# Kernel optimization log

Measured on AMD Instinct MI355X. Metric: run time of the kernel, lower is better.

Reference implementation:

```python
import jax, jax.numpy as jnp
import numpy as np

# Mamba-1.4B-like dims
BATCH, SEQ, HID = 1, 2048, 2048
INTER, STATE, DT_RANK, KCONV = 4096, 16, 128, 4


def setup_inputs() -> dict:
    key = jax.random.key(0)
    ks = jax.random.split(key, 8)
    f = jnp.float32
    return {
        "input_states": jax.random.normal(ks[0], (BATCH, SEQ, HID), f),
        "in_proj_w": jax.random.normal(ks[1], (HID, 2 * INTER), f) * (HID ** -0.5),
        "conv_w": jax.random.normal(ks[2], (INTER, 1, KCONV), f) * (KCONV ** -0.5),  # (O, I/groups=1, K) depthwise
        "conv_b": jnp.zeros((INTER,), f),
        "x_proj_w": jax.random.normal(ks[3], (INTER, DT_RANK + 2 * STATE), f) * (INTER ** -0.5),
        "dt_proj_w": jax.random.normal(ks[4], (DT_RANK, INTER), f) * (DT_RANK ** -0.5),
        "dt_proj_b": jax.random.normal(ks[5], (INTER,), f) * 0.1,
        "A_log": jnp.log(jnp.broadcast_to(jnp.arange(1, STATE + 1, dtype=f), (INTER, STATE))),
        "D": jnp.ones((INTER,), f),
        "out_proj_w": jax.random.normal(ks[6], (INTER, HID), f) * (INTER ** -0.5),
    }


def _mamba_forward(input_states, in_proj_w, conv_w, conv_b, x_proj_w,
                   dt_proj_w, dt_proj_b, A_log, D, out_proj_w):
    Bsz, L, _ = input_states.shape
    Idim, _, K = conv_w.shape
    N = A_log.shape[1]
    R = dt_proj_w.shape[0]

    proj = input_states @ in_proj_w                       # (B, L, 2I)
    hidden, gate = jnp.split(proj, 2, axis=-1)            # each (B, L, I)

    # depthwise causal conv over sequence (pad K-1, keep first L outputs)
    xc = jnp.swapaxes(hidden, 1, 2)                       # (B, I, L)
    xc = jax.lax.conv_general_dilated(
        xc, conv_w, window_strides=(1,), padding=((K - 1, K - 1),),
        feature_group_count=Idim)
    xc = xc[:, :, :L] + conv_b[None, :, None]
    u = jax.nn.silu(jnp.swapaxes(xc, 1, 2))               # (B, L, I)

    # input-dependent SSM params
    ssm_in = u @ x_proj_w                                 # (B, L, R + 2N)
    dt_in, Bc, Cc = jnp.split(ssm_in, [R, R + N], axis=-1)
    dt = jax.nn.softplus(dt_in @ dt_proj_w + dt_proj_b)   # (B, L, I)
    A = -jnp.exp(A_log)                                   # (I, N)

    def step(state, xs):
        dt_t, B_t, C_t, u_t = xs                          # (B,I) (B,N) (B,N) (B,I)
        dA = jnp.exp(dt_t[:, :, None] * A[None])          # (B, I, N)
        state = state * dA + (dt_t * u_t)[:, :, None] * B_t[:, None, :]
        y_t = jnp.einsum('bin,bn->bi', state, C_t)
        return state, y_t

    xs = (jnp.swapaxes(dt, 0, 1), jnp.swapaxes(Bc, 0, 1),
          jnp.swapaxes(Cc, 0, 1), jnp.swapaxes(u, 0, 1))
    state0 = jnp.zeros((Bsz, Idim, N), dt.dtype)
    _, ys = jax.lax.scan(step, state0, xs)                # (L, B, I)
    y = jnp.swapaxes(ys, 0, 1)                            # (B, L, I)

    y = (y + u * D) * jax.nn.silu(gate)
    return y @ out_proj_w                                 # (B, L, H)


def reference(input_states, in_proj_w, conv_w, conv_b, x_proj_w,
              dt_proj_w, dt_proj_b, A_log, D, out_proj_w):
    return _mamba_forward(input_states, in_proj_w, conv_w, conv_b, x_proj_w,
                          dt_proj_w, dt_proj_b, A_log, D, out_proj_w)
```

## Files before the change

kernel.cpp:

```cpp
#include <hip/hip_runtime.h>
#include <stdint.h>

#define LSEQ 2048
#define HID  2048
#define IDIM 4096
#define NSTATE 16
#define RRANK 128
#define GDIM 160

#define GCHUNK 64
#define TCHUNK (LSEQ / GCHUNK)

typedef _Float16 f16x8 __attribute__((ext_vector_type(8)));
typedef _Float16 f16x2 __attribute__((ext_vector_type(2)));
typedef float f32x4 __attribute__((ext_vector_type(4)));

#define GLOAD_LDS16(g, l) __builtin_amdgcn_global_load_lds( \
    (const __attribute__((address_space(1))) void*)(g),     \
    (__attribute__((address_space(3))) void*)(l), 16, 0, 0)

__device__ __forceinline__ float softplus_f(float x) {
    if (x > 20.f) return x;
    return log1pf(__expf(x));
}
__device__ __forceinline__ float silu_f(float x) {
    return x / (1.f + __expf(-x));
}

__device__ __forceinline__ void transpose_tile(const float* __restrict__ in,
                                               _Float16* __restrict__ out,
                                               int R, int C, int tr, int tc,
                                               _Float16 (*tile)[66], int t) {
    const int c0 = tc * 64, r0 = tr * 64;
    const int tx = t & 15, ty = t >> 4;
    const int ox = t & 7, oy = t >> 3;
    const bool full = (c0 + 64 <= C) && (r0 + 64 <= R);
    if (full) {
        #pragma unroll
        for (int j = 0; j < 4; ++j) {
            int r = ty + j * 16;
            float4 v = *(const float4*)(in + (long)(r0 + r) * C + c0 + tx * 4);
            tile[r][tx * 4 + 0] = (_Float16)v.x;
            tile[r][tx * 4 + 1] = (_Float16)v.y;
            tile[r][tx * 4 + 2] = (_Float16)v.z;
            tile[r][tx * 4 + 3] = (_Float16)v.w;
        }
        __syncthreads();
        #pragma unroll
        for (int j = 0; j < 2; ++j) {
            int c = oy + j * 32;
            f16x8 v;
            #pragma unroll
            for (int e = 0; e < 8; ++e) v[e] = tile[ox * 8 + e][c];
            *(f16x8*)(out + (long)(c0 + c) * R + r0 + ox * 8) = v;
        }
    } else {
        #pragma unroll
        for (int j = 0; j < 4; ++j) {
            int r = ty + j * 16;
            #pragma unroll
            for (int e = 0; e < 4; ++e) {
                int c = c0 + tx * 4 + e;
                float v = (r0 + r < R && c < C) ? in[(long)(r0 + r) * C + c] : 0.f;
                tile[r][tx * 4 + e] = (_Float16)v;
            }
        }
        __syncthreads();
        #pragma unroll
        for (int j = 0; j < 2; ++j) {
            int c = c0 + oy + j * 32;
            if (c < C) {
                #pragma unroll
                for (int e = 0; e < 8; ++e) {
                    int r = r0 + ox * 8 + e;
                    if (r < R) out[(long)c * R + r] = tile[ox * 8 + e][oy + j * 32];
                }
            }
        }
    }
}

__global__ __launch_bounds__(256)
void prep_kernel(const float* __restrict__ x_in, const float* __restrict__ w_in,
                 const float* __restrict__ xw, const float* __restrict__ dtw,
                 const float* __restrict__ ow,
                 _Float16* __restrict__ Xf, _Float16* __restrict__ Wt1,
                 _Float16* __restrict__ Wt2, _Float16* __restrict__ Wt3,
                 _Float16* __restrict__ Wt4) {
    __shared__ _Float16 tile[64][66];
    int b = blockIdx.x;
    if (b < 4096) { transpose_tile(w_in, Wt1, HID, 2 * IDIM, b / 128, b % 128, tile, threadIdx.x); return; }
    b -= 4096;
    if (b < 1024) {
        long base = (long)b * 4096 + threadIdx.x * 16;
        #pragma unroll
        for (int h = 0; h < 2; ++h) {
            float4 a = *(const float4*)(x_in + base + h * 8);
            float4 c = *(const float4*)(x_in + base + h * 8 + 4);
            f16x8 v;
            v[0] = (_Float16)a.x; v[1] = (_Float16)a.y; v[2] = (_Float16)a.z; v[3] = (_Float16)a.w;
            v[4] = (_Float16)c.x; v[5] = (_Float16)c.y; v[6] = (_Float16)c.z; v[7] = (_Float16)c.w;
            *(f16x8*)(Xf + base + h * 8) = v;
        }
        return;
    }
    b -= 1024;
    if (b < 192) { transpose_tile(xw, Wt2, IDIM, GDIM, b / 3, b % 3, tile, threadIdx.x); return; }
    b -= 192;
    if (b < 128) { transpose_tile(dtw, Wt3, RRANK, IDIM, b / 64, b % 64, tile, threadIdx.x); return; }
    b -= 128;
    transpose_tile(ow, Wt4, IDIM, HID, b / 32, b % 32, tile, threadIdx.x);
}

#define BM 128
#define BK 64

template <typename CT, bool SOFTPLUS>
__device__ __forceinline__
void gemm_core(const _Float16* __restrict__ A, const _Float16* __restrict__ Bt,
               CT* __restrict__ C, int M, int N, int K, int kc,
               const float* __restrict__ bias,
               _Float16* __restrict__ As, _Float16* __restrict__ Bs,
               int m0, int n0, int zz) {
    const int t = threadIdx.x;
    const int wave = t >> 6;
    const int lane = t & 63;
    const int wm = wave >> 1, wn = wave & 1;
    const int lrow = lane & 15;
    const int quad = lane >> 4;
    const int sw8 = (lrow & 7) * 8;

    f32x4 acc[4][4];
    #pragma unroll
    for (int mi = 0; mi < 4; ++mi)
        #pragma unroll
        for (int ni = 0; ni < 4; ++ni)
            #pragma unroll
            for (int r = 0; r < 4; ++r)
                acc[mi][ni][r] = 0.f;

    const int k_begin = zz * kc;
    const _Float16* pA[4];
    const _Float16* pB[4];
    #pragma unroll
    for (int j = 0; j < 4; ++j) {
        int s = j * 256 + t;
        int row = s >> 3;
        int ch = (s & 7) ^ (row & 7);
        pA[j] = A + (long)(m0 + row) * K + ch * 8 + k_begin;
        pB[j] = Bt + (long)(n0 + row) * K + ch * 8 + k_begin;
    }

    for (int kk = 0; kk < kc; kk += BK) {
        #pragma unroll
        for (int j = 0; j < 4; ++j) {
            GLOAD_LDS16(pA[j], As + (j * 256 + wave * 64) * 8);
            pA[j] += BK;
            GLOAD_LDS16(pB[j], Bs + (j * 256 + wave * 64) * 8);
            pB[j] += BK;
        }
        __syncthreads();

        #pragma unroll
        for (int h = 0; h < 2; ++h) {
            const int qoff = (h * 32 + quad * 8) ^ sw8;
            f16x8 af[4], bf[4];
            #pragma unroll
            for (int mi = 0; mi < 4; ++mi)
                af[mi] = *(const f16x8*)(As + (wm * 64 + mi * 16 + lrow) * BK + qoff);
            #pragma unroll
            for (int ni = 0; ni < 4; ++ni)
                bf[ni] = *(const f16x8*)(Bs + (wn * 64 + ni * 16 + lrow) * BK + qoff);
            #pragma unroll
            for (int mi = 0; mi < 4; ++mi)
                #pragma unroll
                for (int ni = 0; ni < 4; ++ni)
                    acc[mi][ni] = __builtin_amdgcn_mfma_f32_16x16x32_f16(af[mi], bf[ni], acc[mi][ni], 0, 0, 0);
        }
        __syncthreads();
    }

    CT* Cz = C + (long)zz * M * N;
    #pragma unroll
    for (int mi = 0; mi < 4; ++mi) {
        #pragma unroll
        for (int ni = 0; ni < 4; ++ni) {
            int col = n0 + wn * 64 + ni * 16 + lrow;
            if (col < N) {
                float bv = SOFTPLUS ? bias[col] : 0.f;
                #pragma unroll
                for (int r = 0; r < 4; ++r) {
                    int row = m0 + wm * 64 + mi * 16 + quad * 4 + r;
                    float v = acc[mi][ni][r];
                    if (SOFTPLUS) v = softplus_f(v + bv);
                    Cz[(long)row * N + col] = (CT)v;
                }
            }
        }
    }
}

template <typename CT, bool SOFTPLUS>
__global__ __launch_bounds__(256)
void gemm_bt_kernel(const _Float16* __restrict__ A, const _Float16* __restrict__ Bt,
                    CT* __restrict__ C, int M, int N, int K, int kc,
                    const float* __restrict__ bias) {
    __shared__ _Float16 As[BM * BK];
    __shared__ _Float16 Bs[128 * BK];
    gemm_core<CT, SOFTPLUS>(A, Bt, C, M, N, K, kc, bias, As, Bs,
                            blockIdx.y * BM, blockIdx.x * 128, blockIdx.z);
}

template <typename CT>
__device__ __forceinline__
void gemm256_core(const _Float16* __restrict__ A, const _Float16* __restrict__ Bt,
                  CT* __restrict__ C, int M, int N, int K, int kc,
                  int m0, int n0, int zz, _Float16* __restrict__ sm) {
    const int t = threadIdx.x;
    const int wave = t >> 6, lane = t & 63;
    const int wm = wave >> 2, wn = wave & 3;
    const int lrow = lane & 15, quad = lane >> 4;
    const int ns = kc >> 5;

    const int l0 = t >> 3;
    const int e  = (t & 7) ^ (l0 & 7);
    const int sp = e >> 2, sc = e & 3;
    const int rowA = 2 * l0 + sp;
    const _Float16* gA0 = A  + (size_t)(m0 + rowA) * K + (size_t)zz * kc + sc * 8;
    const _Float16* gA1 = gA0 + (size_t)128 * K;
    const _Float16* gB0 = Bt + (size_t)(n0 + rowA) * K + (size_t)zz * kc + sc * 8;
    const _Float16* gB1 = gB0 + (size_t)128 * K;

    _Float16* const bsm = sm + 32768;
    const int dA = wave * 512;

    f32x4 acc[8][4];
    #pragma unroll
    for (int mi = 0; mi < 8; ++mi)
        #pragma unroll
        for (int ni = 0; ni < 4; ++ni)
            #pragma unroll
            for (int r = 0; r < 4; ++r) acc[mi][ni][r] = 0.f;

    #define ISSUE_SLICE(slot) do {                                          \
        _Float16* as_ = sm  + (slot) * 8192;                                \
        _Float16* bs_ = bsm + (slot) * 8192;                                \
        GLOAD_LDS16(gA0, as_ + dA);                                         \
        GLOAD_LDS16(gA1, as_ + 4096 + dA);                                  \
        GLOAD_LDS16(gB0, bs_ + dA);                                         \
        GLOAD_LDS16(gB1, bs_ + 4096 + dA);                                  \
        gA0 += 32; gA1 += 32; gB0 += 32; gB1 += 32;                         \
    } while (0)

    ISSUE_SLICE(0); ISSUE_SLICE(1); ISSUE_SLICE(2);
    asm volatile("s_waitcnt vmcnt(8)" ::: "memory");
    __builtin_amdgcn_s_barrier();
    __builtin_amdgcn_sched_barrier(0);

    const int hl = lrow >> 1;
    const int koff = ((quad + 4 * (lrow & 1)) ^ hl) * 8;
    const int arow0 = wm * 4096 + hl * 64 + koff;
    const int brow0 = wn * 2048 + hl * 64 + koff;

    for (int s2 = 0; s2 < ns; ++s2) {
        const _Float16* as_ = sm  + (s2 & 3) * 8192;
        const _Float16* bs_ = bsm + (s2 & 3) * 8192;
        if (s2 + 3 < ns) ISSUE_SLICE((s2 + 3) & 3);
        __builtin_amdgcn_sched_barrier(0);

        f16x8 af0[4], bf[4];
        #pragma unroll
        for (int mi = 0; mi < 4; ++mi)
            af0[mi] = *(const f16x8*)(as_ + arow0 + mi * 512);
        #pragma unroll
        for (int ni = 0; ni < 4; ++ni)
            bf[ni] = *(const f16x8*)(bs_ + brow0 + ni * 512);

        __builtin_amdgcn_s_setprio(1);
        #pragma unroll
        for (int mi = 0; mi < 4; ++mi)
            #pragma unroll
            for (int ni = 0; ni < 4; ++ni)
                acc[mi][ni] = __builtin_amdgcn_mfma_f32_16x16x32_f16(af0[mi], bf[ni], acc[mi][ni], 0, 0, 0);
        __builtin_amdgcn_s_setprio(0);
        __builtin_amdgcn_sched_barrier(0);

        f16x8 af1[4];
        #pragma unroll
        for (int mi = 0; mi < 4; ++mi)
            af1[mi] = *(const f16x8*)(as_ + arow0 + (mi + 4) * 512);

        __builtin_amdgcn_s_setprio(1);
        #pragma unroll
        for (int mi = 0; mi < 4; ++mi)
            #pragma unroll
            for (int ni = 0; ni < 4; ++ni)
                acc[mi + 4][ni] = __builtin_amdgcn_mfma_f32_16x16x32_f16(af1[mi], bf[ni], acc[mi + 4][ni], 0, 0, 0);
        __builtin_amdgcn_s_setprio(0);

        if (s2 + 1 < ns) {
            if (s2 + 4 <= ns)      asm volatile("s_waitcnt vmcnt(8)" ::: "memory");
            else if (s2 + 3 == ns) asm volatile("s_waitcnt vmcnt(4)" ::: "memory");
            else                   asm volatile("s_waitcnt vmcnt(0)" ::: "memory");
            __builtin_amdgcn_s_barrier();
            __builtin_amdgcn_sched_barrier(0);
        }
    }
    #undef ISSUE_SLICE

    CT* Cz = C + (size_t)zz * ((size_t)M * N);
    const int crow = m0 + wm * 128 + quad * 4;
    const int ccol = n0 + wn * 64 + lrow;
    #pragma unroll
    for (int mi = 0; mi < 8; ++mi)
        #pragma unroll
        for (int ni = 0; ni < 4; ++ni)
            #pragma unroll
            for (int r = 0; r < 4; ++r)
                Cz[(size_t)(crow + mi * 16 + r) * N + ccol + ni * 16] = (CT)acc[mi][ni][r];
}

template <typename CT>
__global__ __launch_bounds__(512, 2)
void gemm256_kernel(const _Float16* __restrict__ A, const _Float16* __restrict__ Bt,
                    CT* __restrict__ C, int M, int N, int K, int kc) {
    __shared__ _Float16 sm[65536];
    int nb = gridDim.x * gridDim.y * gridDim.z;
    int f0 = blockIdx.x + gridDim.x * (blockIdx.y + gridDim.y * blockIdx.z);
    int cpx = nb >> 3;
    int f = (f0 & 7) * cpx + (f0 >> 3);
    int bx = f % gridDim.x;
    int r2 = f / gridDim.x;
    int by = r2 % gridDim.y;
    int bz = r2 / gridDim.y;
    gemm256_core<CT>(A, Bt, C, M, N, K, kc, by * 256, bx * 256, bz, sm);
}

__global__ __launch_bounds__(512, 2)
void inproj256_kernel(const _Float16* __restrict__ Xf, const _Float16* __restrict__ Wt1,
                      _Float16* __restrict__ proj) {
    __shared__ _Float16 sm[65536];
    int b = blockIdx.x;
    int f = (b & 7) * 32 + (b >> 3);
    gemm256_core<_Float16>(Xf, Wt1, proj, LSEQ, 2 * IDIM, HID, HID,
                           (f >> 5) * 256, (f & 31) * 256, 0, sm);
}

__global__ void xproj_reduce_kernel(const float* __restrict__ part, float* __restrict__ ssm,
                                    _Float16* __restrict__ dtin) {
    int idx = blockIdx.x * 256 + threadIdx.x;
    if (idx >= LSEQ * GDIM) return;
    int t = idx / GDIM;
    int c = idx - t * GDIM;
    float v = 0.f;
    #pragma unroll
    for (int k = 0; k < 8; ++k)
        v += part[((long)k * LSEQ + t) * 256 + c];
    ssm[idx] = v;
    if (c < RRANK) dtin[t * RRANK + c] = (_Float16)v;
}

__global__ void opart_reduce_kernel(const _Float16* __restrict__ part, float* __restrict__ out) {
    long base = ((long)blockIdx.x * 256 + threadIdx.x) * 32;
    const long SL = (long)LSEQ * HID;
    #pragma unroll
    for (int j = 0; j < 4; ++j) {
        f16x8 a = *(const f16x8*)(part + base + j * 8);
        f16x8 b = *(const f16x8*)(part + SL + base + j * 8);
        f16x8 c = *(const f16x8*)(part + 2 * SL + base + j * 8);
        f16x8 d = *(const f16x8*)(part + 3 * SL + base + j * 8);
        float4 o0 = make_float4((float)a[0] + (float)b[0] + (float)c[0] + (float)d[0],
                                (float)a[1] + (float)b[1] + (float)c[1] + (float)d[1],
                                (float)a[2] + (float)b[2] + (float)c[2] + (float)d[2],
                                (float)a[3] + (float)b[3] + (float)c[3] + (float)d[3]);
        float4 o1 = make_float4((float)a[4] + (float)b[4] + (float)c[4] + (float)d[4],
                                (float)a[5] + (float)b[5] + (float)c[5] + (float)d[5],
                                (float)a[6] + (float)b[6] + (float)c[6] + (float)d[6],
                                (float)a[7] + (float)b[7] + (float)c[7] + (float)d[7]);
        *(float4*)(out + base + j * 8) = o0;
        *(float4*)(out + base + j * 8 + 4) = o1;
    }
}

__global__ void conv_silu_kernel(const _Float16* __restrict__ proj, const float* __restrict__ w,
                                 const float* __restrict__ b, _Float16* __restrict__ u16) {
    int idx = blockIdx.x * 256 + threadIdx.x;
    int i0 = (idx & 511) * 8;
    int t0 = (idx >> 9) * 4;
    f16x8 r[7];
    #pragma unroll
    for (int k = 0; k < 7; ++k) {
        int tt = t0 - 3 + k;
        if (tt >= 0) r[k] = *(const f16x8*)(proj + (long)tt * (2 * IDIM) + i0);
        else         r[k] = f16x8{0,0,0,0,0,0,0,0};
    }
    float4 wv[8]; float bb[8];
    #pragma unroll
    for (int j = 0; j < 8; ++j) { wv[j] = ((const float4*)w)[i0 + j]; bb[j] = b[i0 + j]; }
    #pragma unroll
    for (int tt = 0; tt < 4; ++tt) {
        f16x8 res;
        #pragma unroll
        for (int j = 0; j < 8; ++j) {
            float a = bb[j] + (float)r[tt][j] * wv[j].x + (float)r[tt+1][j] * wv[j].y
                            + (float)r[tt+2][j] * wv[j].z + (float)r[tt+3][j] * wv[j].w;
            res[j] = (_Float16)(a / (1.f + __expf(-a)));
        }
        *(f16x8*)(u16 + (long)(t0 + tt) * IDIM + i0) = res;
    }
}

__global__ __launch_bounds__(256)
void scan_pass1_kernel(const _Float16* __restrict__ dtf, const float* __restrict__ ssm,
                       const _Float16* __restrict__ u16, const float* __restrict__ A_log,
                       _Float16* __restrict__ Pc, _Float16* __restrict__ Sc) {
    const int c = blockIdx.y;
    const int i0 = (blockIdx.x * 256 + threadIdx.x) * 2;

    __shared__ float Bs[TCHUNK * 16];
    for (int idx = threadIdx.x; idx < TCHUNK * 16; idx += 256) {
        int t = idx >> 4, n = idx & 15;
        Bs[idx] = ssm[(c * TCHUNK + t) * GDIM + RRANK + n];
    }
    __syncthreads();

    float A[2][16];
    #pragma unroll
    for (int ch = 0; ch < 2; ++ch) {
        const float4* Ap = (const float4*)(A_log + (long)(i0 + ch) * 16);
        #pragma unroll
        for (int q = 0; q < 4; ++q) {
            float4 v = Ap[q];
            A[ch][q * 4 + 0] = -__expf(v.x);
            A[ch][q * 4 + 1] = -__expf(v.y);
            A[ch][q * 4 + 2] = -__expf(v.z);
            A[ch][q * 4 + 3] = -__expf(v.w);
        }
    }

    float s[2][16];
    float sumdt[2] = {0.f, 0.f};
    #pragma unroll
    for (int ch = 0; ch < 2; ++ch)
        #pragma unroll
        for (int n = 0; n < 16; ++n) s[ch][n] = 0.f;

    long base = (long)c * TCHUNK * IDIM + i0;
    for (int t = 0; t < TCHUNK; ++t) {
        f16x2 dt2 = *(const f16x2*)(dtf + base + (long)t * IDIM);
        f16x2 u2  = *(const f16x2*)(u16 + base + (long)t * IDIM);
        #pragma unroll
        for (int ch = 0; ch < 2; ++ch) {
            float dt = (float)dt2[ch];
            float dtu = dt * (float)u2[ch];
            sumdt[ch] += dt;
            #pragma unroll
            for (int n = 0; n < 16; ++n) {
                float dA = __expf(dt * A[ch][n]);
                s[ch][n] = s[ch][n] * dA + dtu * Bs[t * 16 + n];
            }
        }
    }

    long o = ((long)c * IDIM + i0) * 16;
    #pragma unroll
    for (int ch = 0; ch < 2; ++ch) {
        #pragma unroll
        for (int q = 0; q < 2; ++q) {
            f16x8 pv, sv;
            #pragma unroll
            for (int e = 0; e < 8; ++e) {
                pv[e] = (_Float16)__expf(A[ch][q * 8 + e] * sumdt[ch]);
                sv[e] = (_Float16)s[ch][q * 8 + e];
            }
            *(f16x8*)(Pc + o + ch * 16 + q * 8) = pv;
            *(f16x8*)(Sc + o + ch * 16 + q * 8) = sv;
        }
    }
}

__global__ void scan_combine_kernel(const _Float16* __restrict__ Pc, _Float16* __restrict__ ScInit) {
    int tid = blockIdx.x * 256 + threadIdx.x;
    const long stride = (long)IDIM * 16;
    const long off = (long)tid * 2;
    f16x2 p4[4], s4[4];
    #pragma unroll
    for (int k = 0; k < 4; ++k) {
        p4[k] = *(const f16x2*)(Pc + (long)k * stride + off);
        s4[k] = *(const f16x2*)(ScInit + (long)k * stride + off);
    }
    float c0 = 0.f, c1 = 0.f;
    for (int g = 0; g < GCHUNK / 4; ++g) {
        f16x2 pc[4], sc[4];
        #pragma unroll
        for (int k = 0; k < 4; ++k) { pc[k] = p4[k]; sc[k] = s4[k]; }
        if (g + 1 < GCHUNK / 4) {
            #pragma unroll
            for (int k = 0; k < 4; ++k) {
                long o2 = (long)((g + 1) * 4 + k) * stride + off;
                p4[k] = *(const f16x2*)(Pc + o2);
                s4[k] = *(const f16x2*)(ScInit + o2);
            }
        }
        #pragma unroll
        for (int k = 0; k < 4; ++k) {
            long o = (long)(g * 4 + k) * stride + off;
            *(f16x2*)(ScInit + o) = f16x2{(_Float16)c0, (_Float16)c1};
            c0 = c0 * (float)pc[k][0] + (float)sc[k][0];
            c1 = c1 * (float)pc[k][1] + (float)sc[k][1];
        }
    }
}

__global__ __launch_bounds__(256)
void scan_pass3_kernel(const _Float16* __restrict__ dtf, const float* __restrict__ ssm,
                       const _Float16* __restrict__ u16, const _Float16* __restrict__ proj,
                       const float* __restrict__ A_log, const float* __restrict__ Dp,
                       const _Float16* __restrict__ Init, _Float16* __restrict__ y16) {
    const int c = blockIdx.y;
    const int i0 = (blockIdx.x * 256 + threadIdx.x) * 2;

    __shared__ float Bs[TCHUNK * 16];
    __shared__ float Cs[TCHUNK * 16];
    for (int idx = threadIdx.x; idx < TCHUNK * 16; idx += 256) {
        int t = idx >> 4, n = idx & 15;
        Bs[idx] = ssm[(c * TCHUNK + t) * GDIM + RRANK + n];
        Cs[idx] = ssm[(c * TCHUNK + t) * GDIM + RRANK + NSTATE + n];
    }
    __syncthreads();

    float A[2][16];
    #pragma unroll
    for (int ch = 0; ch < 2; ++ch) {
        const float4* Ap = (const float4*)(A_log + (long)(i0 + ch) * 16);
        #pragma unroll
        for (int q = 0; q < 4; ++q) {
            float4 v = Ap[q];
            A[ch][q * 4 + 0] = -__expf(v.x);
            A[ch][q * 4 + 1] = -__expf(v.y);
            A[ch][q * 4 + 2] = -__expf(v.z);
            A[ch][q * 4 + 3] = -__expf(v.w);
        }
    }
    float2 Dv = *(const float2*)(Dp + i0);

    float s[2][16];
    {
        long o = ((long)c * IDIM + i0) * 16;
        #pragma unroll
        for (int ch = 0; ch < 2; ++ch)
            #pragma unroll
            for (int q = 0; q < 2; ++q) {
                f16x8 v = *(const f16x8*)(Init + o + ch * 16 + q * 8);
                #pragma unroll
                for (int e = 0; e < 8; ++e) s[ch][q * 8 + e] = (float)v[e];
            }
    }

    long base = (long)c * TCHUNK * IDIM + i0;
    for (int t = 0; t < TCHUNK; ++t) {
        f16x2 dt2 = *(const f16x2*)(dtf + base + (long)t * IDIM);
        f16x2 u2  = *(const f16x2*)(u16 + base + (long)t * IDIM);
        int tg = c * TCHUNK + t;
        f16x2 g2 = *(const f16x2*)(proj + (long)tg * (2 * IDIM) + IDIM + i0);
        f16x2 res;
        #pragma unroll
        for (int ch = 0; ch < 2; ++ch) {
            float dt = (float)dt2[ch];
            float uv = (float)u2[ch];
            float dtu = dt * uv;
            float y = 0.f;
            #pragma unroll
            for (int n = 0; n < 16; ++n) {
                float dA = __expf(dt * A[ch][n]);
                s[ch][n] = s[ch][n] * dA + dtu * Bs[t * 16 + n];
                y += s[ch][n] * Cs[t * 16 + n];
            }
            float g = (float)g2[ch];
            float Dch = ch ? Dv.y : Dv.x;
            res[ch] = (_Float16)((y + uv * Dch) * silu_f(g));
        }
        *(f16x2*)(y16 + base + (long)t * IDIM) = res;
    }
}

extern "C" void kernel_launch(void* const* d_in, const int* in_sizes, int n_in,
                              void* d_out, int out_size, void* d_ws, size_t ws_size,
                              hipStream_t stream) {
    const float* x_in  = (const float*)d_in[0];
    const float* w_in  = (const float*)d_in[1];
    const float* cw    = (const float*)d_in[2];
    const float* cb    = (const float*)d_in[3];
    const float* xw    = (const float*)d_in[4];
    const float* dtw   = (const float*)d_in[5];
    const float* dtb   = (const float*)d_in[6];
    const float* alog  = (const float*)d_in[7];
    const float* Dp    = (const float*)d_in[8];
    const float* ow    = (const float*)d_in[9];
    float* out = (float*)d_out;

    char* p = (char*)d_ws;
    auto alloc = [&](size_t bytes) { char* r = p; p += (bytes + 255) & ~255ull; return r; };
    _Float16* Xf    = (_Float16*)alloc((size_t)LSEQ * HID * 2);
    _Float16* Wt1   = (_Float16*)alloc((size_t)2 * IDIM * HID * 2);
    _Float16* proj  = (_Float16*)alloc((size_t)LSEQ * 2 * IDIM * 2);
    _Float16* u16   = (_Float16*)alloc((size_t)LSEQ * IDIM * 2);
    _Float16* Wt2   = (_Float16*)alloc((size_t)256 * IDIM * 2);
    float*    ssm   = (float*)alloc((size_t)LSEQ * GDIM * 4);
    _Float16* dtin  = (_Float16*)alloc((size_t)LSEQ * RRANK * 2);
    _Float16* Wt3   = (_Float16*)alloc((size_t)IDIM * RRANK * 2);
    _Float16* dtf   = (_Float16*)alloc((size_t)LSEQ * IDIM * 2);
    _Float16* Wt4   = (_Float16*)alloc((size_t)HID * IDIM * 2);
    _Float16* y16   = (_Float16*)alloc((size_t)LSEQ * IDIM * 2);

    float* xpart = (float*)Wt1;
    _Float16* Pc = (_Float16*)Wt1;
    _Float16* Sc = Pc + (size_t)GCHUNK * IDIM * 16;
    _Float16* opart = (_Float16*)Wt1;

    prep_kernel<<<7488, 256, 0, stream>>>(x_in, w_in, xw, dtw, ow,
                                          Xf, Wt1, Wt2, Wt3, Wt4);
    inproj256_kernel<<<256, 512, 0, stream>>>(Xf, Wt1, proj);
    conv_silu_kernel<<<(LSEQ / 4) * (IDIM / 8) / 256, 256, 0, stream>>>(proj, cw, cb, u16);
    gemm_bt_kernel<float, false><<<dim3(2, LSEQ / BM, 8), 256, 0, stream>>>(
        u16, Wt2, xpart, LSEQ, 256, IDIM, IDIM / 8, nullptr);
    xproj_reduce_kernel<<<(LSEQ * GDIM + 255) / 256, 256, 0, stream>>>(xpart, ssm, dtin);
    gemm_bt_kernel<_Float16, true><<<dim3(IDIM / 128, LSEQ / BM, 1), 256, 0, stream>>>(
        dtin, Wt3, dtf, LSEQ, IDIM, RRANK, RRANK, dtb);
    scan_pass1_kernel<<<dim3(IDIM / 512, GCHUNK), 256, 0, stream>>>(
        dtf, ssm, u16, alog, Pc, Sc);
    scan_combine_kernel<<<(IDIM * NSTATE / 2) / 256, 256, 0, stream>>>(Pc, Sc);
    scan_pass3_kernel<<<dim3(IDIM / 512, GCHUNK), 256, 0, stream>>>(
        dtf, ssm, u16, proj, alog, Dp, Sc, y16);
    gemm256_kernel<_Float16><<<dim3(HID / 256, LSEQ / 256, 4), 512, 0, stream>>>(
        y16, Wt4, opart, LSEQ, HID, IDIM, IDIM / 4);
    opart_reduce_kernel<<<(LSEQ * HID / 32) / 256, 256, 0, stream>>>(opart, out);
}
```

Baseline: 458.4 us.

## Move weight transposes into conv kernel; unsplit MFMA loop for out-proj GEMM

```diff
diff --git a/kernel.cpp b/kernel.cpp
--- a/kernel.cpp
+++ b/kernel.cpp
@@ -82,34 +82,21 @@
 
 __global__ __launch_bounds__(256)
 void prep_kernel(const float* __restrict__ x_in, const float* __restrict__ w_in,
-                 const float* __restrict__ xw, const float* __restrict__ dtw,
-                 const float* __restrict__ ow,
-                 _Float16* __restrict__ Xf, _Float16* __restrict__ Wt1,
-                 _Float16* __restrict__ Wt2, _Float16* __restrict__ Wt3,
-                 _Float16* __restrict__ Wt4) {
+                 _Float16* __restrict__ Xf, _Float16* __restrict__ Wt1) {
     __shared__ _Float16 tile[64][66];
     int b = blockIdx.x;
     if (b < 4096) { transpose_tile(w_in, Wt1, HID, 2 * IDIM, b / 128, b % 128, tile, threadIdx.x); return; }
     b -= 4096;
-    if (b < 1024) {
-        long base = (long)b * 4096 + threadIdx.x * 16;
-        #pragma unroll
-        for (int h = 0; h < 2; ++h) {
-            float4 a = *(const float4*)(x_in + base + h * 8);
-            float4 c = *(const float4*)(x_in + base + h * 8 + 4);
-            f16x8 v;
-            v[0] = (_Float16)a.x; v[1] = (_Float16)a.y; v[2] = (_Float16)a.z; v[3] = (_Float16)a.w;
-            v[4] = (_Float16)c.x; v[5] = (_Float16)c.y; v[6] = (_Float16)c.z; v[7] = (_Float16)c.w;
-            *(f16x8*)(Xf + base + h * 8) = v;
-        }
-        return;
-    }
-    b -= 1024;
-    if (b < 192) { transpose_tile(xw, Wt2, IDIM, GDIM, b / 3, b % 3, tile, threadIdx.x); return; }
-    b -= 192;
-    if (b < 128) { transpose_tile(dtw, Wt3, RRANK, IDIM, b / 64, b % 64, tile, threadIdx.x); return; }
-    b -= 128;
-    transpose_tile(ow, Wt4, IDIM, HID, b / 32, b % 32, tile, threadIdx.x);
+    long base = (long)b * 4096 + threadIdx.x * 16;
+    #pragma unroll
+    for (int h = 0; h < 2; ++h) {
+        float4 a = *(const float4*)(x_in + base + h * 8);
+        float4 c = *(const float4*)(x_in + base + h * 8 + 4);
+        f16x8 v;
+        v[0] = (_Float16)a.x; v[1] = (_Float16)a.y; v[2] = (_Float16)a.z; v[3] = (_Float16)a.w;
+        v[4] = (_Float16)c.x; v[5] = (_Float16)c.y; v[6] = (_Float16)c.z; v[7] = (_Float16)c.w;
+        *(f16x8*)(Xf + base + h * 8) = v;
+    }
 }
 
 #define BM 128
@@ -211,7 +198,7 @@
                             blockIdx.y * BM, blockIdx.x * 128, blockIdx.z);
 }
 
-template <typename CT>
+template <typename CT, bool SPLIT>
 __device__ __forceinline__
 void gemm256_core(const _Float16* __restrict__ A, const _Float16* __restrict__ Bt,
                   CT* __restrict__ C, int M, int N, int K, int kc,
@@ -268,35 +255,53 @@
         if (s2 + 3 < ns) ISSUE_SLICE((s2 + 3) & 3);
         __builtin_amdgcn_sched_barrier(0);
 
-        f16x8 af0[4], bf[4];
-        #pragma unroll
-        for (int mi = 0; mi < 4; ++mi)
-            af0[mi] = *(const f16x8*)(as_ + arow0 + mi * 512);
-        #pragma unroll
-        for (int ni = 0; ni < 4; ++ni)
-            bf[ni] = *(const f16x8*)(bs_ + brow0 + ni * 512);
-
-        __builtin_amdgcn_s_setprio(1);
-        #pragma unroll
-        for (int mi = 0; mi < 4; ++mi)
+        if constexpr (!SPLIT) {
+            f16x8 af[8], bf[4];
+            #pragma unroll
+            for (int mi = 0; mi < 8; ++mi)
+                af[mi] = *(const f16x8*)(as_ + arow0 + mi * 512);
             #pragma unroll
             for (int ni = 0; ni < 4; ++ni)
-                acc[mi][ni] = __builtin_amdgcn_mfma_f32_16x16x32_f16(af0[mi], bf[ni], acc[mi][ni], 0, 0, 0);
-        __builtin_amdgcn_s_setprio(0);
-        __builtin_amdgcn_sched_barrier(0);
-
-        f16x8 af1[4];
-        #pragma unroll
-        for (int mi = 0; mi < 4; ++mi)
-            af1[mi] = *(const f16x8*)(as_ + arow0 + (mi + 4) * 512);
-
-        __builtin_amdgcn_s_setprio(1);
-        #pragma unroll
-        for (int mi = 0; mi < 4; ++mi)
+                bf[ni] = *(const f16x8*)(bs_ + brow0 + ni * 512);
+
+            __builtin_amdgcn_s_setprio(1);
+            #pragma unroll
+            for (int mi = 0; mi < 8; ++mi)
+                #pragma unroll
+                for (int ni = 0; ni < 4; ++ni)
+                    acc[mi][ni] = __builtin_amdgcn_mfma_f32_16x16x32_f16(af[mi], bf[ni], acc[mi][ni], 0, 0, 0);
+            __builtin_amdgcn_s_setprio(0);
+        } else {
+            f16x8 af0[4], bf[4];
+            #pragma unroll
+            for (int mi = 0; mi < 4; ++mi)
+                af0[mi] = *(const f16x8*)(as_ + arow0 + mi * 512);
             #pragma unroll
             for (int ni = 0; ni < 4; ++ni)
-                acc[mi + 4][ni] = __builtin_amdgcn_mfma_f32_16x16x32_f16(af1[mi], bf[ni], acc[mi + 4][ni], 0, 0, 0);
-        __builtin_amdgcn_s_setprio(0);
+                bf[ni] = *(const f16x8*)(bs_ + brow0 + ni * 512);
+
+            __builtin_amdgcn_s_setprio(1);
+            #pragma unroll
+            for (int mi = 0; mi < 4; ++mi)
+                #pragma unroll
+                for (int ni = 0; ni < 4; ++ni)
+                    acc[mi][ni] = __builtin_amdgcn_mfma_f32_16x16x32_f16(af0[mi], bf[ni], acc[mi][ni], 0, 0, 0);
+            __builtin_amdgcn_s_setprio(0);
+            __builtin_amdgcn_sched_barrier(0);
+
+            f16x8 af1[4];
+            #pragma unroll
+            for (int mi = 0; mi < 4; ++mi)
+                af1[mi] = *(const f16x8*)(as_ + arow0 + (mi + 4) * 512);
+
+            __builtin_amdgcn_s_setprio(1);
+            #pragma unroll
+            for (int mi = 0; mi < 4; ++mi)
+                #pragma unroll
+                for (int ni = 0; ni < 4; ++ni)
+                    acc[mi + 4][ni] = __builtin_amdgcn_mfma_f32_16x16x32_f16(af1[mi], bf[ni], acc[mi + 4][ni], 0, 0, 0);
+            __builtin_amdgcn_s_setprio(0);
+        }
 
         if (s2 + 1 < ns) {
             if (s2 + 4 <= ns)      asm volatile("s_waitcnt vmcnt(8)" ::: "memory");
@@ -333,7 +338,7 @@
     int r2 = f / gridDim.x;
     int by = r2 % gridDim.y;
     int bz = r2 / gridDim.y;
-    gemm256_core<CT>(A, Bt, C, M, N, K, kc, by * 256, bx * 256, bz, sm);
+    gemm256_core<CT, false>(A, Bt, C, M, N, K, kc, by * 256, bx * 256, bz, sm);
 }
 
 __global__ __launch_bounds__(512, 2)
@@ -342,8 +347,8 @@
     __shared__ _Float16 sm[65536];
     int b = blockIdx.x;
     int f = (b & 7) * 32 + (b >> 3);
-    gemm256_core<_Float16>(Xf, Wt1, proj, LSEQ, 2 * IDIM, HID, HID,
-                           (f >> 5) * 256, (f & 31) * 256, 0, sm);
+    gemm256_core<_Float16, true>(Xf, Wt1, proj, LSEQ, 2 * IDIM, HID, HID,
+                                 (f >> 5) * 256, (f & 31) * 256, 0, sm);
 }
 
 __global__ void xproj_reduce_kernel(const float* __restrict__ part, float* __restrict__ ssm,
@@ -382,9 +387,25 @@
     }
 }
 
-__global__ void conv_silu_kernel(const _Float16* __restrict__ proj, const float* __restrict__ w,
-                                 const float* __restrict__ b, _Float16* __restrict__ u16) {
-    int idx = blockIdx.x * 256 + threadIdx.x;
+__global__ __launch_bounds__(256)
+void conv_plus_kernel(const _Float16* __restrict__ proj, const float* __restrict__ w,
+                      const float* __restrict__ b, _Float16* __restrict__ u16,
+                      const float* __restrict__ xw, const float* __restrict__ dtw,
+                      const float* __restrict__ ow,
+                      _Float16* __restrict__ Wt2, _Float16* __restrict__ Wt3,
+                      _Float16* __restrict__ Wt4) {
+    __shared__ _Float16 tile[64][66];
+    int blk = blockIdx.x;
+    if (blk >= 1024) {
+        int b2 = blk - 1024;
+        if (b2 < 192) { transpose_tile(xw, Wt2, IDIM, GDIM, b2 / 3, b2 % 3, tile, threadIdx.x); return; }
+        b2 -= 192;
+        if (b2 < 128) { transpose_tile(dtw, Wt3, RRANK, IDIM, b2 / 64, b2 % 64, tile, threadIdx.x); return; }
+        b2 -= 128;
+        transpose_tile(ow, Wt4, IDIM, HID, b2 / 32, b2 % 32, tile, threadIdx.x);
+        return;
+    }
+    int idx = blk * 256 + threadIdx.x;
     int i0 = (idx & 511) * 8;
     int t0 = (idx >> 9) * 4;
     f16x8 r[7];
@@ -618,10 +639,10 @@
     _Float16* Sc = Pc + (size_t)GCHUNK * IDIM * 16;
     _Float16* opart = (_Float16*)Wt1;
 
-    prep_kernel<<<7488, 256, 0, stream>>>(x_in, w_in, xw, dtw, ow,
-                                          Xf, Wt1, Wt2, Wt3, Wt4);
+    prep_kernel<<<5120, 256, 0, stream>>>(x_in, w_in, Xf, Wt1);
     inproj256_kernel<<<256, 512, 0, stream>>>(Xf, Wt1, proj);
-    conv_silu_kernel<<<(LSEQ / 4) * (IDIM / 8) / 256, 256, 0, stream>>>(proj, cw, cb, u16);
+    conv_plus_kernel<<<1024 + 2368, 256, 0, stream>>>(
+        proj, cw, cb, u16, xw, dtw, ow, Wt2, Wt3, Wt4);
     gemm_bt_kernel<float, false><<<dim3(2, LSEQ / BM, 8), 256, 0, stream>>>(
         u16, Wt2, xpart, LSEQ, 256, IDIM, IDIM / 8, nullptr);
     xproj_reduce_kernel<<<(LSEQ * GDIM + 255) / 256, 256, 0, stream>>>(xpart, ssm, dtin);
```

Measured after the change: 462.1 us. No clear change (+0.8%).

## Use dedicated 128x256-tile out-projection GEMM kernel with higher occupancy

Applied to the files above, without the earlier changes.

```diff
diff --git a/kernel.cpp b/kernel.cpp
--- a/kernel.cpp
+++ b/kernel.cpp
@@ -320,22 +320,6 @@
                 Cz[(size_t)(crow + mi * 16 + r) * N + ccol + ni * 16] = (CT)acc[mi][ni][r];
 }
 
-template <typename CT>
-__global__ __launch_bounds__(512, 2)
-void gemm256_kernel(const _Float16* __restrict__ A, const _Float16* __restrict__ Bt,
-                    CT* __restrict__ C, int M, int N, int K, int kc) {
-    __shared__ _Float16 sm[65536];
-    int nb = gridDim.x * gridDim.y * gridDim.z;
-    int f0 = blockIdx.x + gridDim.x * (blockIdx.y + gridDim.y * blockIdx.z);
-    int cpx = nb >> 3;
-    int f = (f0 & 7) * cpx + (f0 >> 3);
-    int bx = f % gridDim.x;
-    int r2 = f / gridDim.x;
-    int by = r2 % gridDim.y;
-    int bz = r2 / gridDim.y;
-    gemm256_core<CT>(A, Bt, C, M, N, K, kc, by * 256, bx * 256, bz, sm);
-}
-
 __global__ __launch_bounds__(512, 2)
 void inproj256_kernel(const _Float16* __restrict__ Xf, const _Float16* __restrict__ Wt1,
                       _Float16* __restrict__ proj) {
@@ -344,6 +328,116 @@
     int f = (b & 7) * 32 + (b >> 3);
     gemm256_core<_Float16>(Xf, Wt1, proj, LSEQ, 2 * IDIM, HID, HID,
                            (f >> 5) * 256, (f & 31) * 256, 0, sm);
+}
+
+__global__ __launch_bounds__(512, 4)
+void oproj128_kernel(const _Float16* __restrict__ A, const _Float16* __restrict__ Bt,
+                     _Float16* __restrict__ C, int M, int N, int K, int kc) {
+    __shared__ _Float16 sm[24576];
+    int f0 = blockIdx.x + gridDim.x * (blockIdx.y + gridDim.y * blockIdx.z);
+    int f = (f0 & 7) * 64 + (f0 >> 3);
+    int bx = f % 8;
+    int r2 = f / 8;
+    int by = r2 % 16;
+    int bz = r2 / 16;
+    const int m0 = by * 128, n0 = bx * 256, zz = bz;
+
+    const int t = threadIdx.x;
+    const int wave = t >> 6, lane = t & 63;
+    const int wm = wave >> 2, wn = wave & 3;
+    const int lrow = lane & 15, quad = lane >> 4;
+    const int ns = kc >> 5;
+
+    {
+    }
+    const int lA = t >> 3;
+    const int eA = (t & 7) ^ (lA & 7);
+    const int rowA = 2 * lA + (eA >> 2);
+    const _Float16* gA = A + (size_t)(m0 + rowA) * K + (size_t)zz * kc + (eA & 3) * 8;
+    const int lB0 = t >> 3;
+    const int eB0 = (t & 7) ^ (lB0 & 7);
+    const int rowB0 = 2 * lB0 + (eB0 >> 2);
+    const int lB1 = (512 + t) >> 3;
+    const int eB1 = (t & 7) ^ (lB1 & 7);
+    const int rowB1 = 2 * lB1 + (eB1 >> 2);
+    const _Float16* gB0 = Bt + (size_t)(n0 + rowB0) * K + (size_t)zz * kc + (eB0 & 3) * 8;
+    const _Float16* gB1 = Bt + (size_t)(n0 + rowB1) * K + (size_t)zz * kc + (eB1 & 3) * 8;
+
+    _Float16* const bsm = sm + 8192;
+    const int dA = wave * 512;
+
+    f32x4 acc[4][4];
+    #pragma unroll
+    for (int mi = 0; mi < 4; ++mi)
+        #pragma unroll
+        for (int ni = 0; ni < 4; ++ni)
+            #pragma unroll
+            for (int r = 0; r < 4; ++r) acc[mi][ni][r] = 0.f;
+
+    #define OISSUE(slot) do {                                               \
+        _Float16* as_ = sm  + (slot) * 4096;                                \
+        _Float16* bs_ = bsm + (slot) * 8192;                                \
+        GLOAD_LDS16(gA,  as_ + dA);                                         \
+        GLOAD_LDS16(gB0, bs_ + dA);                                         \
+        GLOAD_LDS16(gB1, bs_ + 4096 + dA);                                  \
+        gA += 32; gB0 += 32; gB1 += 32;                                     \
+    } while (0)
+
+    OISSUE(0); OISSUE(1);
+    asm volatile("s_waitcnt vmcnt(3)" ::: "memory");
+    __builtin_amdgcn_s_barrier();
+    __builtin_amdgcn_sched_barrier(0);
+
+    const int hl = lrow >> 1;
+    const int koff = ((quad + 4 * (lrow & 1)) ^ hl) * 8;
+    const int arow0 = wm * 2048 + hl * 64 + koff;
+    const int brow0 = wn * 2048 + hl * 64 + koff;
+
+    for (int s = 0; s < ns; ++s) {
+        const _Float16* as_ = sm  + (s & 1) * 4096;
+        const _Float16* bs_ = bsm + (s & 1) * 8192;
+
+        f16x8 af[4], bf[4];
+        #pragma unroll
+        for (int mi = 0; mi < 4; ++mi)
+            af[mi] = *(const f16x8*)(as_ + arow0 + mi * 512);
+        #pragma unroll
+        for (int ni = 0; ni < 4; ++ni)
+            bf[ni] = *(const f16x8*)(bs_ + brow0 + ni * 512);
+
+        __builtin_amdgcn_s_setprio(1);
+        #pragma unroll
+        for (int mi = 0; mi < 4; ++mi)
+            #pragma unroll
+            for (int ni = 0; ni < 4; ++ni)
+                acc[mi][ni] = __builtin_amdgcn_mfma_f32_16x16x32_f16(af[mi], bf[ni], acc[mi][ni], 0, 0, 0);
+        __builtin_amdgcn_s_setprio(0);
+
+        if (s + 1 < ns) {
+            __builtin_amdgcn_s_barrier();
+            __builtin_amdgcn_sched_barrier(0);
+            if (s + 2 < ns) {
+                OISSUE((s + 2) & 1);
+                asm volatile("s_waitcnt vmcnt(3)" ::: "memory");
+            } else {
+                asm volatile("s_waitcnt vmcnt(0)" ::: "memory");
+            }
+            __builtin_amdgcn_s_barrier();
+            __builtin_amdgcn_sched_barrier(0);
+        }
+    }
+    #undef OISSUE
+
+    _Float16* Cz = C + (size_t)zz * ((size_t)M * N);
+    const int crow = m0 + wm * 64 + quad * 4;
+    const int ccol = n0 + wn * 64 + lrow;
+    #pragma unroll
+    for (int mi = 0; mi < 4; ++mi)
+        #pragma unroll
+        for (int ni = 0; ni < 4; ++ni)
+            #pragma unroll
+            for (int r = 0; r < 4; ++r)
+                Cz[(size_t)(crow + mi * 16 + r) * N + ccol + ni * 16] = (_Float16)acc[mi][ni][r];
 }
 
 __global__ void xproj_reduce_kernel(const float* __restrict__ part, float* __restrict__ ssm,
@@ -632,7 +726,7 @@
     scan_combine_kernel<<<(IDIM * NSTATE / 2) / 256, 256, 0, stream>>>(Pc, Sc);
     scan_pass3_kernel<<<dim3(IDIM / 512, GCHUNK), 256, 0, stream>>>(
         dtf, ssm, u16, proj, alog, Dp, Sc, y16);
-    gemm256_kernel<_Float16><<<dim3(HID / 256, LSEQ / 256, 4), 512, 0, stream>>>(
+    oproj128_kernel<<<dim3(HID / 256, LSEQ / 128, 4), 512, 0, stream>>>(
         y16, Wt4, opart, LSEQ, HID, IDIM, IDIM / 4);
     opart_reduce_kernel<<<(LSEQ * HID / 32) / 256, 256, 0, stream>>>(opart, out);
 }
```

Measured after the change: 474.5 us. 3.5% more time.
